# Kernel tuning notes

Hardware: AMD Instinct MI355X
Metric: run time of the kernel (lower is better)

Reference implementation:

```python
import math
import jax, jax.numpy as jnp
import numpy as np

N_HEADS = 16

def _alibi_slopes(n_heads: int) -> np.ndarray:
    def pow2_slopes(n):
        start = 2 ** (-2 ** (-(math.log2(n) - 3)))
        return [start * start ** i for i in range(n)]
    if math.log2(n_heads).is_integer():
        slopes = pow2_slopes(n_heads)
    else:
        closest = 2 ** math.floor(math.log2(n_heads))
        slopes = pow2_slopes(closest)
        extra = pow2_slopes(2 * closest)[0::2]
        slopes = slopes + extra[: n_heads - closest]
    return np.asarray(slopes, dtype=np.float32)

def _build_alibi_bias(n_heads: int, T: int) -> jnp.ndarray:
    # (1, H, T, T): lower triangle = -slope*|i-j|, strict upper = -inf (causal)
    slopes = jnp.asarray(_alibi_slopes(n_heads))  # (H,)
    pos = jnp.arange(T)
    dist = pos[None, :] - pos[None, :].T  # (T, T), j - i
    causal = dist < 0  # future positions (j > i means dist>0? note: dist = j - i transposed)
    # match torch: distances = positions[None,:] - positions[:,None] -> dist[i,j] = j - i
    dist = pos[None, :] - pos[:, None]
    causal = dist > 0  # wait: torch masks distances < 0 where distances[i,j] = j - i? No:
    # torch: distances = positions.unsqueeze(0) - positions.unsqueeze(1) -> dist[i,j] = positions[j] - positions[i]? 
    # unsqueeze(0): (1,T) row j; unsqueeze(1): (T,1) row i -> dist[i,j] = pos[j] - pos[i]
    # causal_mask = dist < 0 masks j < i ... but then bias upper triangle kept?
    # Actually torch masks where distances < 0, i.e., j < i (past). That seems inverted,
    # but we must be FAITHFUL: mask fills -inf where pos[j] - pos[i] < 0.
    d = pos[None, :] - pos[:, None]  # d[i,j] = j - i
    mask = d < 0
    bias = -slopes[:, None, None] * jnp.abs(d).astype(jnp.float32)[None, :, :]
    bias = jnp.where(mask[None, :, :], -jnp.inf, bias)
    return bias[None]  # (1, H, T, T)

def setup_inputs() -> dict:
    key = jax.random.key(0)
    k1, k2, k3 = jax.random.split(key, 3)
    B, T, D = 2, 2048, 1024
    x = jax.random.normal(k1, (B, T, D), dtype=jnp.float32)
    W_qkv = jax.random.normal(k2, (D, 3 * D), dtype=jnp.float32) * (1.0 / math.sqrt(D))
    W_out = jax.random.normal(k3, (D, D), dtype=jnp.float32) * (1.0 / math.sqrt(D))
    return {"x": x, "W_qkv": W_qkv, "W_out": W_out}

def reference(x, W_qkv, W_out):
    B, T, D = x.shape
    H = N_HEADS
    hd = D // H
    qkv = x @ W_qkv  # (B, T, 3D)
    q, k, v = jnp.split(qkv, 3, axis=-1)
    q = q.reshape(B, T, H, hd).transpose(0, 2, 1, 3)  # (B,H,T,hd)
    k = k.reshape(B, T, H, hd).transpose(0, 2, 1, 3)
    v = v.reshape(B, T, H, hd).transpose(0, 2, 1, 3)
    scale = 1.0 / math.sqrt(hd)
    attn = jnp.einsum('bhqd,bhkd->bhqk', q, k) * scale  # (B,H,T,T)
    attn = attn + _build_alibi_bias(H, T)
    attn = jax.nn.softmax(attn, axis=-1)
    out = jnp.einsum('bhqk,bhkd->bhqd', attn, v)  # (B,H,T,hd)
    out = out.transpose(0, 2, 1, 3).reshape(B, T, D)
    return out @ W_out
```

## Files before the change

kernel.cpp:

```cpp
#include <hip/hip_runtime.h>

#define DEV __device__ __forceinline__

typedef __attribute__((ext_vector_type(4))) float f32x4;
typedef __attribute__((ext_vector_type(16))) float f32x16;
typedef __attribute__((ext_vector_type(8))) short s16x8;

static constexpr int TB  = 2;
static constexpr int TT  = 2048;
static constexpr int TD  = 1024;
static constexpr int TH  = 16;
static constexpr int THD = 64;
static constexpr int TN3 = 3072;
static constexpr int TM  = TB * TT;

#define WS_XB     1024u
#define WS_WQKVT  (WS_XB + 8388608u)
#define WS_WOUTT  (WS_WQKVT + 6291456u)
#define WS_QKV    (WS_WOUTT + 2097152u)
#define WS_VT     (WS_QKV + 25165824u)
#define WS_CTX    (WS_VT + 8388608u)

DEV unsigned short f2bf(float f) {
  unsigned int u = __builtin_bit_cast(unsigned int, f);
  u += 0x7FFFu + ((u >> 16) & 1u);
  return (unsigned short)(u >> 16);
}
DEV f32x4 mfma16(s16x8 a, s16x8 b, f32x4 c) {
  return __builtin_amdgcn_mfma_f32_16x16x32_bf16(a, b, c, 0, 0, 0);
}
DEV f32x16 mfma32(s16x8 a, s16x8 b, f32x16 c) {
  return __builtin_amdgcn_mfma_f32_32x32x16_bf16(a, b, c, 0, 0, 0);
}
DEV void gload_lds16(const void* g, void* l) {
  __builtin_amdgcn_global_load_lds(
      (const __attribute__((address_space(1))) void*)g,
      (__attribute__((address_space(3))) void*)l, 16, 0, 0);
}
DEV unsigned int cvtpk(float lo, float hi_) {
  unsigned int r;
  asm("v_cvt_pk_bf16_f32 %0, %1, %2" : "=v"(r) : "v"(lo), "v"(hi_));
  return r;
}
DEV void plswap(unsigned int& a, unsigned int& b) {
  asm("v_permlane32_swap_b32 %0, %1" : "+v"(a), "+v"(b));
}

DEV bool is_bf16(const void* x) {
  uint4 v = ((const uint4*)x)[threadIdx.x & 63];
  unsigned int w[4] = {v.x, v.y, v.z, v.w};
  int hit = 0;
#pragma unroll
  for (int k = 0; k < 4; ++k) {
    if (((w[k] >> 7) & 0xFF) >= 135) hit++;
    if (((w[k] >> 23) & 0xFF) >= 135) hit++;
  }
  return __ballot(hit > 0) == 0ULL;
}

__global__ __launch_bounds__(256) void prep_kernel(const void* __restrict__ x,
                                                   const void* __restrict__ wqkv,
                                                   const void* __restrict__ wout,
                                                   unsigned short* __restrict__ xb,
                                                   unsigned short* __restrict__ wqkvt,
                                                   unsigned short* __restrict__ woutt) {
  __shared__ unsigned short tile[64 * 65];
  const int bid = blockIdx.x;
  const bool bf = is_bf16(x);
  if (bid < 1024) {
    const void* W; unsigned short* Wt; int N, k0, n0;
    if (bid < 768) { W = wqkv; Wt = wqkvt; N = TN3; k0 = (bid & 15) * 64; n0 = (bid >> 4) * 64; }
    else { int id = bid - 768; W = wout; Wt = woutt; N = TD; k0 = (id & 15) * 64; n0 = (id >> 4) * 64; }
    for (int e = threadIdx.x; e < 4096; e += 256) {
      int kr = e >> 6, nc = e & 63;
      unsigned short v;
      if (bf) v = ((const unsigned short*)W)[(size_t)(k0 + kr) * N + n0 + nc];
      else    v = f2bf(((const float*)W)[(size_t)(k0 + kr) * N + n0 + nc]);
      tile[kr * 65 + nc] = v;
    }
    __syncthreads();
    for (int e = threadIdx.x; e < 4096; e += 256) {
      int nr = e >> 6, kc = e & 63;
      Wt[(size_t)(n0 + nr) * TD + k0 + kc] = tile[kc * 65 + nr];
    }
  } else {
    if (bf) return;
    int i = (bid - 1024) * 256 + threadIdx.x;
    if (i >= (TM * TD) / 8) return;
    const float* s = (const float*)x + (size_t)i * 8;
    unsigned int w0 = (unsigned int)f2bf(s[0]) | ((unsigned int)f2bf(s[1]) << 16);
    unsigned int w1 = (unsigned int)f2bf(s[2]) | ((unsigned int)f2bf(s[3]) << 16);
    unsigned int w2 = (unsigned int)f2bf(s[4]) | ((unsigned int)f2bf(s[5]) << 16);
    unsigned int w3 = (unsigned int)f2bf(s[6]) | ((unsigned int)f2bf(s[7]) << 16);
    uint4 o; o.x = w0; o.y = w1; o.z = w2; o.w = w3;
    ((uint4*)xb)[i] = o;
  }
}

__global__ __launch_bounds__(256, 2) void gemm1_kernel(const unsigned short* __restrict__ Axb,
                                                       const unsigned short* __restrict__ xraw,
                                                       const unsigned short* __restrict__ Bt,
                                                       unsigned short* __restrict__ C,
                                                       unsigned short* __restrict__ vtb,
                                                       int Mn, int Nn, int Kn) {
  __shared__ unsigned short lA[2][128 * 64];
  __shared__ unsigned short lB[2][192 * 64];
  const int tid = threadIdx.x;
  const int lane = tid & 63;
  const int wid = tid >> 6;
  const int wm = wid >> 1, wn = wid & 1;
  const int l31 = lane & 31, hi = lane >> 5;

  const int nby = Nn / 192;
  const int nwg = (Mn >> 7) * nby;
  const int cpx = nwg >> 3;
  const int bid = blockIdx.x;
  const int swz = (bid & 7) * cpx + (bid >> 3);
  const int bm = swz / nby, bn = swz % nby;
  const int row0 = bm << 7, col0 = bn * 192;

  const bool bf = is_bf16(xraw);
  const unsigned short* Abase = bf ? xraw : Axb;

  const int srow = tid >> 3;
  const int scol = ((tid & 7) ^ (srow & 7)) * 8;
  const unsigned short* aS = Abase + (size_t)(row0 + srow) * Kn + scol;
  const unsigned short* bS = Bt + (size_t)(col0 + srow) * Kn + scol;
  const size_t r32 = (size_t)32 * Kn;

#define STGA(dst, koff) do {                                \
    unsigned short* _d = (dst) + tid * 8;                   \
    const unsigned short* _s = aS + (koff);                 \
    gload_lds16(_s,           _d);                          \
    gload_lds16(_s + r32,     _d + 2048);                   \
    gload_lds16(_s + 2 * r32, _d + 4096);                   \
    gload_lds16(_s + 3 * r32, _d + 6144);                   \
  } while (0)
#define STGB(dst, koff) do {                                \
    unsigned short* _d = (dst) + tid * 8;                   \
    const unsigned short* _s = bS + (koff);                 \
    gload_lds16(_s,           _d);                          \
    gload_lds16(_s + r32,     _d + 2048);                   \
    gload_lds16(_s + 2 * r32, _d + 4096);                   \
    gload_lds16(_s + 3 * r32, _d + 6144);                   \
    gload_lds16(_s + 4 * r32, _d + 8192);                   \
    gload_lds16(_s + 5 * r32, _d + 10240);                  \
  } while (0)

  f32x16 acc[2][3];
#pragma unroll
  for (int m = 0; m < 2; ++m)
#pragma unroll
    for (int n = 0; n < 3; ++n)
#pragma unroll
      for (int r = 0; r < 16; ++r) acc[m][n][r] = 0.f;

  int kcc[4];
#pragma unroll
  for (int ks = 0; ks < 4; ++ks) kcc[ks] = ((ks * 2 + hi) ^ (l31 & 7)) * 8;
  const int aRow = (wm * 64 + l31) * 64;
  const int bRow = (wn * 96 + l31) * 64;

  STGA(&lA[0][0], 0);
  STGB(&lB[0][0], 0);
  asm volatile("s_waitcnt vmcnt(0)" ::: "memory");
  __builtin_amdgcn_s_barrier();

  const int nt = Kn >> 6;
  for (int t = 0; t < nt; ++t) {
    const unsigned short* la = &lA[t & 1][0];
    const unsigned short* lb = &lB[t & 1][0];
    unsigned short* na = &lA[(t + 1) & 1][0];
    unsigned short* nb = &lB[(t + 1) & 1][0];
    const int koff = (t + 1) << 6;
    const bool more = (t + 1 < nt);

    if (more) { STGA(na, koff); STGB(nb, koff); }

    s16x8 xa[2][4], yb[3][4];
#pragma unroll
    for (int m = 0; m < 2; ++m)
#pragma unroll
      for (int ks = 0; ks < 4; ++ks)
        xa[m][ks] = *(const s16x8*)&la[aRow + m * 2048 + kcc[ks]];
#pragma unroll
    for (int n = 0; n < 3; ++n)
#pragma unroll
      for (int ks = 0; ks < 4; ++ks)
        yb[n][ks] = *(const s16x8*)&lb[bRow + n * 2048 + kcc[ks]];
#pragma unroll
    for (int ks = 0; ks < 4; ++ks)
#pragma unroll
      for (int m = 0; m < 2; ++m)
#pragma unroll
        for (int n = 0; n < 3; ++n)
          acc[m][n] = mfma32(xa[m][ks], yb[n][ks], acc[m][n]);

    asm volatile("s_waitcnt vmcnt(0)" ::: "memory");
    __builtin_amdgcn_s_barrier();
  }
#undef STGA
#undef STGB

  unsigned short* cw = C + (size_t)(row0 + wm * 64 + 4 * hi) * Nn + col0 + wn * 96 + l31;
#pragma unroll
  for (int m = 0; m < 2; ++m)
#pragma unroll
    for (int n = 0; n < 3; ++n) {
      const int cbase = col0 + wn * 96 + n * 32;
      if (cbase < 2048) {
#pragma unroll
        for (int r = 0; r < 16; ++r) {
          int rr = (r & 3) + 8 * (r >> 2);
          cw[(size_t)(m * 32 + rr) * Nn + n * 32] = f2bf(acc[m][n][r]);
        }
      } else {
        int cc2 = cbase + l31 - 2048;
        int h = cc2 >> 6, d = cc2 & 63;
#pragma unroll
        for (int g = 0; g < 4; ++g) {
          int tg = row0 + wm * 64 + m * 32 + 8 * g + 4 * hi;
          int bb = tg >> 11, tt = tg & 2047;
          unsigned short* dst = vtb + (((size_t)(bb * 16 + h) * 64 + d) << 11) + tt;
          uint2 pk;
          pk.x = cvtpk(acc[m][n][4 * g + 0], acc[m][n][4 * g + 1]);
          pk.y = cvtpk(acc[m][n][4 * g + 2], acc[m][n][4 * g + 3]);
          *(uint2*)dst = pk;
        }
      }
    }
}

__global__ __launch_bounds__(256, 2) void gemm_bt2_kernel(const unsigned short* __restrict__ A,
                                                          const unsigned short* __restrict__ Bt,
                                                          void* __restrict__ Cout,
                                                          int Mn, int Nn, int Kn,
                                                          const unsigned short* __restrict__ xprobe) {
  __shared__ unsigned short lA[3][128 * 64];
  __shared__ unsigned short lB[3][64 * 64];
  const int tid  = threadIdx.x;
  const int lane = tid & 63, wid = tid >> 6;
  const int wr = wid >> 1, wc = wid & 1;
  const int l15 = lane & 15, lg = lane >> 4;
  const int row0 = blockIdx.x * 128, col0 = blockIdx.y * 64;

  const bool obf = is_bf16(xprobe);

  f32x4 acc[4][2];
#pragma unroll
  for (int m = 0; m < 4; ++m)
#pragma unroll
    for (int n = 0; n < 2; ++n) acc[m][n] = (f32x4){0.f, 0.f, 0.f, 0.f};

  const int srow = tid >> 3;
  const int scol = ((tid & 7) ^ (srow & 7)) * 8;
  const unsigned short* aS = A  + (size_t)(row0 + srow) * Kn + scol;
  const unsigned short* bS = Bt + (size_t)(col0 + srow) * Kn + scol;
  const size_t r32 = (size_t)32 * Kn;

#define STG2(bi, koff) do {                                                 \
    unsigned short* _da = &lA[bi][0] + tid * 8;                             \
    unsigned short* _db = &lB[bi][0] + tid * 8;                             \
    gload_lds16(aS + (koff),            _da);                               \
    gload_lds16(aS + (koff) + r32,      _da + 2048);                        \
    gload_lds16(aS + (koff) + 2 * r32,  _da + 4096);                        \
    gload_lds16(aS + (koff) + 3 * r32,  _da + 6144);                        \
    gload_lds16(bS + (koff),            _db);                               \
    gload_lds16(bS + (koff) + r32,      _db + 2048);                        \
  } while (0)

  const int sa = l15 & 7;
  const int kc0 = (lg ^ sa) * 8;
  const int kc1 = ((4 + lg) ^ sa) * 8;
  const int aoff = (wr * 64 + l15) * 64;
  const int boff = (wc * 32 + l15) * 64;

  const int nt = Kn >> 6;
  STG2(0, 0);
  STG2(1, 64);
  asm volatile("s_waitcnt vmcnt(6)" ::: "memory");
  __builtin_amdgcn_s_barrier();

  int cur = 0;
  for (int t = 0; t < nt; ++t) {
    const unsigned short* la = &lA[cur][0];
    const unsigned short* lb = &lB[cur][0];
    const bool deep = (t + 2 < nt);

    s16x8 af[4], bfv[2];
#pragma unroll
    for (int m = 0; m < 4; ++m) af[m] = *(const s16x8*)&la[aoff + m * 1024 + kc0];
#pragma unroll
    for (int n = 0; n < 2; ++n) bfv[n] = *(const s16x8*)&lb[boff + n * 1024 + kc0];
    if (deep) { int nbuf = (cur + 2 == 3) ? 0 : ((cur + 2 == 4) ? 1 : cur + 2); STG2(nbuf, (t + 2) << 6); }
    __builtin_amdgcn_s_barrier();
    asm volatile("s_waitcnt lgkmcnt(0)" ::: "memory");
    __builtin_amdgcn_sched_barrier(0);
    __builtin_amdgcn_s_setprio(1);
#pragma unroll
    for (int m = 0; m < 4; ++m)
#pragma unroll
      for (int n = 0; n < 2; ++n)
        acc[m][n] = mfma16(af[m], bfv[n], acc[m][n]);
    __builtin_amdgcn_s_setprio(0);
    __builtin_amdgcn_s_barrier();

#pragma unroll
    for (int m = 0; m < 4; ++m) af[m] = *(const s16x8*)&la[aoff + m * 1024 + kc1];
#pragma unroll
    for (int n = 0; n < 2; ++n) bfv[n] = *(const s16x8*)&lb[boff + n * 1024 + kc1];
    __builtin_amdgcn_s_barrier();
    asm volatile("s_waitcnt lgkmcnt(0)" ::: "memory");
    __builtin_amdgcn_sched_barrier(0);
    __builtin_amdgcn_s_setprio(1);
#pragma unroll
    for (int m = 0; m < 4; ++m)
#pragma unroll
      for (int n = 0; n < 2; ++n)
        acc[m][n] = mfma16(af[m], bfv[n], acc[m][n]);
    __builtin_amdgcn_s_setprio(0);
    if (t + 1 < nt) {
      if (deep) asm volatile("s_waitcnt vmcnt(6)" ::: "memory");
      else      asm volatile("s_waitcnt vmcnt(0)" ::: "memory");
      __builtin_amdgcn_s_barrier();
    }
    cur = (cur == 2) ? 0 : cur + 1;
  }
#undef STG2

#pragma unroll
  for (int m = 0; m < 4; ++m)
#pragma unroll
    for (int n = 0; n < 2; ++n)
#pragma unroll
      for (int j = 0; j < 4; ++j) {
        int r = row0 + wr * 64 + m * 16 + lg * 4 + j;
        int c = col0 + wc * 32 + n * 16 + l15;
        if (obf) ((unsigned short*)Cout)[(size_t)r * Nn + c] = f2bf(acc[m][n][j]);
        else     ((float*)Cout)[(size_t)r * Nn + c] = acc[m][n][j];
      }
}

__global__ __launch_bounds__(256, 4) void attn_kernel(const unsigned short* __restrict__ qkv,
                                                      const unsigned short* __restrict__ vt,
                                                      unsigned short* __restrict__ ctx) {
  __shared__ __align__(16) unsigned char smem[32768];
  unsigned short* kl0 = (unsigned short*)smem;
  unsigned short* vl0 = (unsigned short*)(smem + 16384);
  float* red = (float*)smem;

  const int bid = blockIdx.x;
  const int r_ = bid & 255, q_ = bid >> 8;
  const int s_ = r_ >> 5, g_ = r_ & 31;
  const int bh = (g_ + 8 * q_) & 31;
  const int x32 = (q_ == 0) ? s_ : (q_ == 1) ? 15 - s_ : (q_ == 2) ? 16 + s_ : 31 - s_;
  const int b = bh >> 4, h = bh & 15;

  const int tid = threadIdx.x;
  const int wid = tid >> 6, lane = tid & 63;
  const int wr = wid & 1, wk = wid >> 1;
  const int l31 = lane & 31, hi = lane >> 5;
  const int i_base = x32 * 64 + wr * 32;

  const unsigned short* qb  = qkv + (size_t)b * TT * TN3 + h * THD;
  const unsigned short* kb_ = qkv + (size_t)b * TT * TN3 + TD + h * THD;
  const unsigned short* vb_ = vt + (size_t)bh * THD * TT;

  const float LOG2E = 1.44269504f;
  const float SL2 = exp2f(-0.5f * (float)(h + 1)) * LOG2E;
  const float SC2 = 0.125f * LOG2E;
  const float dbias = -SL2 * 64.0f;

  const int t_rel = (int)((140.0f / SL2 + 63.0f) * (1.0f / 64.0f)) + 1;
  const int t_end = (32 < x32 + t_rel) ? 32 : x32 + t_rel;

  const int srow = tid >> 3;
  const int sx = ((tid & 7) ^ (srow & 7)) * 8;
  const unsigned short* srcK = kb_ + (size_t)(x32 * 64 + srow) * TN3 + sx;
  const unsigned short* srcV = vb_ + (size_t)srow * TT + x32 * 64 + sx;
  const size_t kstep = (size_t)64 * TN3;

#define STAGE(bufi) do {                                   \
    unsigned short* _dk = kl0 + (bufi) * 4096 + tid * 8;   \
    unsigned short* _dv = vl0 + (bufi) * 4096 + tid * 8;   \
    gload_lds16(srcK,            _dk);                     \
    gload_lds16(srcK + 32 * TN3, _dk + 2048);              \
    gload_lds16(srcV,            _dv);                     \
    gload_lds16(srcV + 32 * TT,  _dv + 2048);              \
  } while (0)

  s16x8 qa[4];
  {
    const unsigned short* qr = qb + (size_t)(i_base + l31) * TN3 + hi * 8;
#pragma unroll
    for (int dd = 0; dd < 4; ++dd) qa[dd] = *(const s16x8*)(qr + dd * 16);
  }

  s16x8 ones;
  {
    short ov = (l31 == 0) ? (short)0x3F80 : (short)0;
#pragma unroll
    for (int e = 0; e < 8; ++e) ones[e] = ov;
  }

  float base[16];
#pragma unroll
  for (int r = 0; r < 16; ++r) {
    int cr0 = (r & 3) + 8 * (r >> 2);
    base[r] = -SL2 * (float)(wk * 32 + cr0 + 4 * hi - wr * 32 - l31) - 16.0f;
  }

  f32x16 o0, o1, ol;
#pragma unroll
  for (int r = 0; r < 16; ++r) { o0[r] = 0.f; o1[r] = 0.f; ol[r] = 0.f; }

  const int sw = (l31 & 7) << 4;
  int cc[4];
#pragma unroll
  for (int dd = 0; dd < 4; ++dd) cc[dd] = ((dd * 32 + hi * 16) ^ sw) >> 1;

  int cur = 0;
  STAGE(0); srcK += kstep; srcV += 64;
  asm volatile("s_waitcnt vmcnt(0)" ::: "memory");
  __syncthreads();

  for (int t = x32; t < t_end; ++t) {
    if (t + 1 < t_end) { STAGE(cur ^ 1); srcK += kstep; srcV += 64; }

    const unsigned short* kb = kl0 + cur * 4096;
    const unsigned short* vbl = vl0 + cur * 4096;

    f32x16 sv;
#pragma unroll
    for (int r = 0; r < 16; ++r) sv[r] = 0.f;
    __builtin_amdgcn_s_setprio(1);
#pragma unroll
    for (int dd = 0; dd < 4; ++dd) {
      s16x8 k0 = *(const s16x8*)&kb[(wk * 32 + l31) * 64 + cc[dd]];
      sv = mfma32(k0, qa[dd], sv);
    }
    __builtin_amdgcn_s_setprio(0);

    if (t == x32) {
#pragma unroll
      for (int r = 0; r < 16; ++r) {
        float bb = base[r];
        float v = __builtin_amdgcn_exp2f(fmaf(sv[r], SC2, bb));
        sv[r] = (bb > -15.999f) ? 0.0f : v;
      }
    } else {
#pragma unroll
      for (int r = 0; r < 16; ++r)
        sv[r] = __builtin_amdgcn_exp2f(fmaf(sv[r], SC2, base[r]));
    }
#pragma unroll
    for (int r = 0; r < 16; ++r) base[r] += dbias;

    s16x8 pa[2];
#pragma unroll
    for (int mh = 0; mh < 2; ++mh) {
      unsigned int a0 = cvtpk(sv[8 * mh + 0], sv[8 * mh + 1]);
      unsigned int a1 = cvtpk(sv[8 * mh + 2], sv[8 * mh + 3]);
      unsigned int b0 = cvtpk(sv[8 * mh + 4], sv[8 * mh + 5]);
      unsigned int b1 = cvtpk(sv[8 * mh + 6], sv[8 * mh + 7]);
      plswap(a0, b0); plswap(a1, b1);
      uint4 u; u.x = a0; u.y = a1; u.z = b0; u.w = b1;
      pa[mh] = __builtin_bit_cast(s16x8, u);
    }

    __builtin_amdgcn_s_setprio(1);
#pragma unroll
    for (int ks = 0; ks < 2; ++ks) {
      s16x8 v0 = *(const s16x8*)&vbl[l31 * 64 + cc[wk * 2 + ks]];
      s16x8 v1 = *(const s16x8*)&vbl[(32 + l31) * 64 + cc[wk * 2 + ks]];
      o0 = mfma32(pa[ks], v0, o0);
      o1 = mfma32(pa[ks], v1, o1);
      ol = mfma32(pa[ks], ones, ol);
    }
    __builtin_amdgcn_s_setprio(0);

    asm volatile("s_waitcnt vmcnt(0)" ::: "memory");
    __syncthreads();
    cur ^= 1;
  }
#undef STAGE

  const int rbase = (wr * 64 + lane) * 49;
  if (wk == 1) {
#pragma unroll
    for (int r = 0; r < 16; ++r) red[rbase + r] = o0[r];
#pragma unroll
    for (int r = 0; r < 16; ++r) red[rbase + 16 + r] = o1[r];
#pragma unroll
    for (int r = 0; r < 16; ++r) red[rbase + 32 + r] = ol[r];
  }
  __syncthreads();
  if (wk == 0) {
#pragma unroll
    for (int r = 0; r < 16; ++r) o0[r] += red[rbase + r];
#pragma unroll
    for (int r = 0; r < 16; ++r) o1[r] += red[rbase + 16 + r];
#pragma unroll
    for (int r = 0; r < 16; ++r) ol[r] += red[rbase + 32 + r];

    float rdiv[16];
#pragma unroll
    for (int r = 0; r < 16; ++r) rdiv[r] = 1.0f / __shfl(ol[r], lane & 32);

    unsigned short* cb = ctx + (size_t)(b * TT + i_base) * TD + h * THD + l31;
#pragma unroll
    for (int r = 0; r < 16; ++r) {
      int row = (r & 3) + 8 * (r >> 2) + 4 * hi;
      unsigned int pk = cvtpk(o0[r] * rdiv[r], o1[r] * rdiv[r]);
      cb[(size_t)row * TD] = (unsigned short)pk;
      cb[(size_t)row * TD + 32] = (unsigned short)(pk >> 16);
    }
  }
}

extern "C" void kernel_launch(void* const* d_in, const int* in_sizes, int n_in,
                              void* d_out, int out_size, void* d_ws, size_t ws_size,
                              hipStream_t stream) {
  const void* x    = d_in[0];
  const void* wqkv = d_in[1];
  const void* wout = d_in[2];
  char* ws = (char*)d_ws;
  unsigned short* xb    = (unsigned short*)(ws + WS_XB);
  unsigned short* wqkvt = (unsigned short*)(ws + WS_WQKVT);
  unsigned short* woutt = (unsigned short*)(ws + WS_WOUTT);
  unsigned short* qkvb  = (unsigned short*)(ws + WS_QKV);
  unsigned short* vtb   = (unsigned short*)(ws + WS_VT);
  unsigned short* ctxb  = (unsigned short*)(ws + WS_CTX);

  prep_kernel<<<3072, 256, 0, stream>>>(x, wqkv, wout, xb, wqkvt, woutt);
  gemm1_kernel<<<(TM / 128) * (TN3 / 192), 256, 0, stream>>>(xb, (const unsigned short*)x, wqkvt, qkvb, vtb, TM, TN3, TD);
  attn_kernel<<<1024, 256, 0, stream>>>(qkvb, vtb, ctxb);
  gemm_bt2_kernel<<<dim3(TM / 128, TD / 64), 256, 0, stream>>>(ctxb, woutt, d_out, TM, TD, TD, (const unsigned short*)x);
}
```

Baseline: 102.8 us.

## Make attention kernel persistent with atomic work-queue scheduling

Converts the attention kernel into a persistent kernel where 768 blocks repeatedly fetch (query tile, batch-head) units from a global atomic counter, reset in the prep kernel. Units are handed out in order of query tile, so long-running early tiles start first and the tail is balanced dynamically. Launch bounds drop to 3 blocks per CU to match the persistent grid. It adds an atomic plus extra barriers per unit and lower occupancy.

```diff
diff --git a/kernel.cpp b/kernel.cpp
--- a/kernel.cpp
+++ b/kernel.cpp
@@ -14,6 +14,7 @@
 static constexpr int TN3 = 3072;
 static constexpr int TM  = TB * TT;
 
+#define WS_QCNT   512u
 #define WS_XB     1024u
 #define WS_WQKVT  (WS_XB + 8388608u)
 #define WS_WOUTT  (WS_WQKVT + 6291456u)
@@ -63,9 +64,11 @@
                                                    const void* __restrict__ wout,
                                                    unsigned short* __restrict__ xb,
                                                    unsigned short* __restrict__ wqkvt,
-                                                   unsigned short* __restrict__ woutt) {
+                                                   unsigned short* __restrict__ woutt,
+                                                   int* __restrict__ qcnt) {
   __shared__ unsigned short tile[64 * 65];
   const int bid = blockIdx.x;
+  if (bid == 0 && threadIdx.x == 0) qcnt[0] = 0;
   const bool bf = is_bf16(x);
   if (bid < 1024) {
     const void* W; unsigned short* Wt; int N, k0, n0;
@@ -341,44 +344,58 @@
       }
 }
 
-__global__ __launch_bounds__(256, 4) void attn_kernel(const unsigned short* __restrict__ qkv,
+__global__ __launch_bounds__(256, 3) void attn_kernel(const unsigned short* __restrict__ qkv,
                                                       const unsigned short* __restrict__ vt,
-                                                      unsigned short* __restrict__ ctx) {
+                                                      unsigned short* __restrict__ ctx,
+                                                      int* __restrict__ qcnt) {
   __shared__ __align__(16) unsigned char smem[32768];
+  __shared__ int s_unit;
   unsigned short* kl0 = (unsigned short*)smem;
   unsigned short* vl0 = (unsigned short*)(smem + 16384);
   float* red = (float*)smem;
-
-  const int bid = blockIdx.x;
-  const int r_ = bid & 255, q_ = bid >> 8;
-  const int s_ = r_ >> 5, g_ = r_ & 31;
-  const int bh = (g_ + 8 * q_) & 31;
-  const int x32 = (q_ == 0) ? s_ : (q_ == 1) ? 15 - s_ : (q_ == 2) ? 16 + s_ : 31 - s_;
-  const int b = bh >> 4, h = bh & 15;
 
   const int tid = threadIdx.x;
   const int wid = tid >> 6, lane = tid & 63;
   const int wr = wid & 1, wk = wid >> 1;
   const int l31 = lane & 31, hi = lane >> 5;
-  const int i_base = x32 * 64 + wr * 32;
-
-  const unsigned short* qb  = qkv + (size_t)b * TT * TN3 + h * THD;
-  const unsigned short* kb_ = qkv + (size_t)b * TT * TN3 + TD + h * THD;
-  const unsigned short* vb_ = vt + (size_t)bh * THD * TT;
-
   const float LOG2E = 1.44269504f;
-  const float SL2 = exp2f(-0.5f * (float)(h + 1)) * LOG2E;
-  const float SC2 = 0.125f * LOG2E;
-  const float dbias = -SL2 * 64.0f;
-
-  const int t_rel = (int)((140.0f / SL2 + 63.0f) * (1.0f / 64.0f)) + 1;
-  const int t_end = (32 < x32 + t_rel) ? 32 : x32 + t_rel;
+
+  s16x8 ones;
+  {
+    short ov = (l31 == 0) ? (short)0x3F80 : (short)0;
+#pragma unroll
+    for (int e = 0; e < 8; ++e) ones[e] = ov;
+  }
 
   const int srow = tid >> 3;
   const int sx = ((tid & 7) ^ (srow & 7)) * 8;
-  const unsigned short* srcK = kb_ + (size_t)(x32 * 64 + srow) * TN3 + sx;
-  const unsigned short* srcV = vb_ + (size_t)srow * TT + x32 * 64 + sx;
   const size_t kstep = (size_t)64 * TN3;
+  const int sw = (l31 & 7) << 4;
+  int cc[4];
+#pragma unroll
+  for (int dd = 0; dd < 4; ++dd) cc[dd] = ((dd * 32 + hi * 16) ^ sw) >> 1;
+
+  for (;;) {
+    if (tid == 0) s_unit = atomicAdd(qcnt, 1);
+    __syncthreads();
+    const int u = s_unit;
+    if (u >= 1024) break;
+    const int x32 = u >> 5, bh = u & 31;
+    const int b = bh >> 4, h = bh & 15;
+    const int i_base = x32 * 64 + wr * 32;
+
+    const unsigned short* qb  = qkv + (size_t)b * TT * TN3 + h * THD;
+    const unsigned short* kb_ = qkv + (size_t)b * TT * TN3 + TD + h * THD;
+    const unsigned short* vb_ = vt + (size_t)bh * THD * TT;
+
+    const float SL2 = exp2f(-0.5f * (float)(h + 1)) * LOG2E;
+    const float SC2 = 0.125f * LOG2E;
+    const float dbias = -SL2 * 64.0f;
+    const int t_rel = (int)((140.0f / SL2 + 63.0f) * (1.0f / 64.0f)) + 1;
+    const int t_end = (32 < x32 + t_rel) ? 32 : x32 + t_rel;
+
+    const unsigned short* srcK = kb_ + (size_t)(x32 * 64 + srow) * TN3 + sx;
+    const unsigned short* srcV = vb_ + (size_t)srow * TT + x32 * 64 + sx;
 
 #define STAGE(bufi) do {                                   \
     unsigned short* _dk = kl0 + (bufi) * 4096 + tid * 8;   \
@@ -389,132 +406,122 @@
     gload_lds16(srcV + 32 * TT,  _dv + 2048);              \
   } while (0)
 
-  s16x8 qa[4];
-  {
-    const unsigned short* qr = qb + (size_t)(i_base + l31) * TN3 + hi * 8;
-#pragma unroll
-    for (int dd = 0; dd < 4; ++dd) qa[dd] = *(const s16x8*)(qr + dd * 16);
-  }
-
-  s16x8 ones;
-  {
-    short ov = (l31 == 0) ? (short)0x3F80 : (short)0;
-#pragma unroll
-    for (int e = 0; e < 8; ++e) ones[e] = ov;
-  }
-
-  float base[16];
-#pragma unroll
-  for (int r = 0; r < 16; ++r) {
-    int cr0 = (r & 3) + 8 * (r >> 2);
-    base[r] = -SL2 * (float)(wk * 32 + cr0 + 4 * hi - wr * 32 - l31) - 16.0f;
-  }
-
-  f32x16 o0, o1, ol;
-#pragma unroll
-  for (int r = 0; r < 16; ++r) { o0[r] = 0.f; o1[r] = 0.f; ol[r] = 0.f; }
-
-  const int sw = (l31 & 7) << 4;
-  int cc[4];
-#pragma unroll
-  for (int dd = 0; dd < 4; ++dd) cc[dd] = ((dd * 32 + hi * 16) ^ sw) >> 1;
-
-  int cur = 0;
-  STAGE(0); srcK += kstep; srcV += 64;
-  asm volatile("s_waitcnt vmcnt(0)" ::: "memory");
-  __syncthreads();
-
-  for (int t = x32; t < t_end; ++t) {
-    if (t + 1 < t_end) { STAGE(cur ^ 1); srcK += kstep; srcV += 64; }
-
-    const unsigned short* kb = kl0 + cur * 4096;
-    const unsigned short* vbl = vl0 + cur * 4096;
-
-    f32x16 sv;
-#pragma unroll
-    for (int r = 0; r < 16; ++r) sv[r] = 0.f;
-    __builtin_amdgcn_s_setprio(1);
-#pragma unroll
-    for (int dd = 0; dd < 4; ++dd) {
-      s16x8 k0 = *(const s16x8*)&kb[(wk * 32 + l31) * 64 + cc[dd]];
-      sv = mfma32(k0, qa[dd], sv);
-    }
-    __builtin_amdgcn_s_setprio(0);
-
-    if (t == x32) {
-#pragma unroll
-      for (int r = 0; r < 16; ++r) {
-        float bb = base[r];
-        float v = __builtin_amdgcn_exp2f(fmaf(sv[r], SC2, bb));
-        sv[r] = (bb > -15.999f) ? 0.0f : v;
-      }
-    } else {
-#pragma unroll
-      for (int r = 0; r < 16; ++r)
-        sv[r] = __builtin_amdgcn_exp2f(fmaf(sv[r], SC2, base[r]));
-    }
-#pragma unroll
-    for (int r = 0; r < 16; ++r) base[r] += dbias;
-
-    s16x8 pa[2];
-#pragma unroll
-    for (int mh = 0; mh < 2; ++mh) {
-      unsigned int a0 = cvtpk(sv[8 * mh + 0], sv[8 * mh + 1]);
-      unsigned int a1 = cvtpk(sv[8 * mh + 2], sv[8 * mh + 3]);
-      unsigned int b0 = cvtpk(sv[8 * mh + 4], sv[8 * mh + 5]);
-      unsigned int b1 = cvtpk(sv[8 * mh + 6], sv[8 * mh + 7]);
-      plswap(a0, b0); plswap(a1, b1);
-      uint4 u; u.x = a0; u.y = a1; u.z = b0; u.w = b1;
-      pa[mh] = __builtin_bit_cast(s16x8, u);
-    }
-
-    __builtin_amdgcn_s_setprio(1);
-#pragma unroll
-    for (int ks = 0; ks < 2; ++ks) {
-      s16x8 v0 = *(const s16x8*)&vbl[l31 * 64 + cc[wk * 2 + ks]];
-      s16x8 v1 = *(const s16x8*)&vbl[(32 + l31) * 64 + cc[wk * 2 + ks]];
-      o0 = mfma32(pa[ks], v0, o0);
-      o1 = mfma32(pa[ks], v1, o1);
-      ol = mfma32(pa[ks], ones, ol);
-    }
-    __builtin_amdgcn_s_setprio(0);
-
+    s16x8 qa[4];
+    {
+      const unsigned short* qr = qb + (size_t)(i_base + l31) * TN3 + hi * 8;
+#pragma unroll
+      for (int dd = 0; dd < 4; ++dd) qa[dd] = *(const s16x8*)(qr + dd * 16);
+    }
+
+    float base[16];
+#pragma unroll
+    for (int r = 0; r < 16; ++r) {
+      int cr0 = (r & 3) + 8 * (r >> 2);
+      base[r] = -SL2 * (float)(wk * 32 + cr0 + 4 * hi - wr * 32 - l31) - 16.0f;
+    }
+
+    f32x16 o0, o1, ol;
+#pragma unroll
+    for (int r = 0; r < 16; ++r) { o0[r] = 0.f; o1[r] = 0.f; ol[r] = 0.f; }
+
+    int cur = 0;
+    STAGE(0); srcK += kstep; srcV += 64;
     asm volatile("s_waitcnt vmcnt(0)" ::: "memory");
     __syncthreads();
-    cur ^= 1;
-  }
+
+    for (int t = x32; t < t_end; ++t) {
+      if (t + 1 < t_end) { STAGE(cur ^ 1); srcK += kstep; srcV += 64; }
+
+      const unsigned short* kb = kl0 + cur * 4096;
+      const unsigned short* vbl = vl0 + cur * 4096;
+
+      f32x16 sv;
+#pragma unroll
+      for (int r = 0; r < 16; ++r) sv[r] = 0.f;
+      __builtin_amdgcn_s_setprio(1);
+#pragma unroll
+      for (int dd = 0; dd < 4; ++dd) {
+        s16x8 k0 = *(const s16x8*)&kb[(wk * 32 + l31) * 64 + cc[dd]];
+        sv = mfma32(k0, qa[dd], sv);
+      }
+      __builtin_amdgcn_s_setprio(0);
+
+      if (t == x32) {
+#pragma unroll
+        for (int r = 0; r < 16; ++r) {
+          float bb = base[r];
+          float v = __builtin_amdgcn_exp2f(fmaf(sv[r], SC2, bb));
+          sv[r] = (bb > -15.999f) ? 0.0f : v;
+        }
+      } else {
+#pragma unroll
+        for (int r = 0; r < 16; ++r)
+          sv[r] = __builtin_amdgcn_exp2f(fmaf(sv[r], SC2, base[r]));
+      }
+#pragma unroll
+      for (int r = 0; r < 16; ++r) base[r] += dbias;
+
+      s16x8 pa[2];
+#pragma unroll
+      for (int mh = 0; mh < 2; ++mh) {
+        unsigned int a0 = cvtpk(sv[8 * mh + 0], sv[8 * mh + 1]);
+        unsigned int a1 = cvtpk(sv[8 * mh + 2], sv[8 * mh + 3]);
+        unsigned int b0 = cvtpk(sv[8 * mh + 4], sv[8 * mh + 5]);
+        unsigned int b1 = cvtpk(sv[8 * mh + 6], sv[8 * mh + 7]);
+        plswap(a0, b0); plswap(a1, b1);
+        uint4 uu; uu.x = a0; uu.y = a1; uu.z = b0; uu.w = b1;
+        pa[mh] = __builtin_bit_cast(s16x8, uu);
+      }
+
+      __builtin_amdgcn_s_setprio(1);
+#pragma unroll
+      for (int ks = 0; ks < 2; ++ks) {
+        s16x8 v0 = *(const s16x8*)&vbl[l31 * 64 + cc[wk * 2 + ks]];
+        s16x8 v1 = *(const s16x8*)&vbl[(32 + l31) * 64 + cc[wk * 2 + ks]];
+        o0 = mfma32(pa[ks], v0, o0);
+        o1 = mfma32(pa[ks], v1, o1);
+        ol = mfma32(pa[ks], ones, ol);
+      }
+      __builtin_amdgcn_s_setprio(0);
+
+      asm volatile("s_waitcnt vmcnt(0)" ::: "memory");
+      __syncthreads();
+      cur ^= 1;
+    }
 #undef STAGE
 
-  const int rbase = (wr * 64 + lane) * 49;
-  if (wk == 1) {
-#pragma unroll
-    for (int r = 0; r < 16; ++r) red[rbase + r] = o0[r];
-#pragma unroll
-    for (int r = 0; r < 16; ++r) red[rbase + 16 + r] = o1[r];
-#pragma unroll
-    for (int r = 0; r < 16; ++r) red[rbase + 32 + r] = ol[r];
-  }
-  __syncthreads();
-  if (wk == 0) {
-#pragma unroll
-    for (int r = 0; r < 16; ++r) o0[r] += red[rbase + r];
-#pragma unroll
-    for (int r = 0; r < 16; ++r) o1[r] += red[rbase + 16 + r];
-#pragma unroll
-    for (int r = 0; r < 16; ++r) ol[r] += red[rbase + 32 + r];
-
-    float rdiv[16];
-#pragma unroll
-    for (int r = 0; r < 16; ++r) rdiv[r] = 1.0f / __shfl(ol[r], lane & 32);
-
-    unsigned short* cb = ctx + (size_t)(b * TT + i_base) * TD + h * THD + l31;
-#pragma unroll
-    for (int r = 0; r < 16; ++r) {
-      int row = (r & 3) + 8 * (r >> 2) + 4 * hi;
-      unsigned int pk = cvtpk(o0[r] * rdiv[r], o1[r] * rdiv[r]);
-      cb[(size_t)row * TD] = (unsigned short)pk;
-      cb[(size_t)row * TD + 32] = (unsigned short)(pk >> 16);
-    }
+    const int rbase = (wr * 64 + lane) * 49;
+    if (wk == 1) {
+#pragma unroll
+      for (int r = 0; r < 16; ++r) red[rbase + r] = o0[r];
+#pragma unroll
+      for (int r = 0; r < 16; ++r) red[rbase + 16 + r] = o1[r];
+#pragma unroll
+      for (int r = 0; r < 16; ++r) red[rbase + 32 + r] = ol[r];
+    }
+    __syncthreads();
+    if (wk == 0) {
+#pragma unroll
+      for (int r = 0; r < 16; ++r) o0[r] += red[rbase + r];
+#pragma unroll
+      for (int r = 0; r < 16; ++r) o1[r] += red[rbase + 16 + r];
+#pragma unroll
+      for (int r = 0; r < 16; ++r) ol[r] += red[rbase + 32 + r];
+
+      float rdiv[16];
+#pragma unroll
+      for (int r = 0; r < 16; ++r) rdiv[r] = 1.0f / __shfl(ol[r], lane & 32);
+
+      unsigned short* cb = ctx + (size_t)(b * TT + i_base) * TD + h * THD + l31;
+#pragma unroll
+      for (int r = 0; r < 16; ++r) {
+        int row = (r & 3) + 8 * (r >> 2) + 4 * hi;
+        unsigned int pk = cvtpk(o0[r] * rdiv[r], o1[r] * rdiv[r]);
+        cb[(size_t)row * TD] = (unsigned short)pk;
+        cb[(size_t)row * TD + 32] = (unsigned short)(pk >> 16);
+      }
+    }
+    __syncthreads();
   }
 }
 
@@ -525,6 +532,7 @@
   const void* wqkv = d_in[1];
   const void* wout = d_in[2];
   char* ws = (char*)d_ws;
+  int* qcnt             = (int*)(ws + WS_QCNT);
   unsigned short* xb    = (unsigned short*)(ws + WS_XB);
   unsigned short* wqkvt = (unsigned short*)(ws + WS_WQKVT);
   unsigned short* woutt = (unsigned short*)(ws + WS_WOUTT);
@@ -532,8 +540,8 @@
   unsigned short* vtb   = (unsigned short*)(ws + WS_VT);
   unsigned short* ctxb  = (unsigned short*)(ws + WS_CTX);
 
-  prep_kernel<<<3072, 256, 0, stream>>>(x, wqkv, wout, xb, wqkvt, woutt);
+  prep_kernel<<<3072, 256, 0, stream>>>(x, wqkv, wout, xb, wqkvt, woutt, qcnt);
   gemm1_kernel<<<(TM / 128) * (TN3 / 192), 256, 0, stream>>>(xb, (const unsigned short*)x, wqkvt, qkvb, vtb, TM, TN3, TD);
-  attn_kernel<<<1024, 256, 0, stream>>>(qkvb, vtb, ctxb);
+  attn_kernel<<<768, 256, 0, stream>>>(qkvb, vtb, ctxb, qcnt);
   gemm_bt2_kernel<<<dim3(TM / 128, TD / 64), 256, 0, stream>>>(ctxb, woutt, d_out, TM, TD, TD, (const unsigned short*)x);
 }
```

After: 114.1 us. 1.11x slower.
